# Performance work log

Hardware: AMD Instinct MI355X
Metric: run time of the kernel (lower is better)

Reference implementation:

```python
import jax, jax.numpy as jnp
import numpy as np


def _he_scale(k, shape, fan_in):
    return jax.random.normal(k, shape, dtype=jnp.float32) * np.sqrt(2.0 / fan_in).astype(np.float32)


def setup_inputs() -> dict:
    key = jax.random.key(0)
    kx, kt, kp, kg, kf = jax.random.split(key, 5)
    B, H, W, C, D = 4, 64, 64, 256, 128
    x = jax.random.normal(kx, (B, H, W, C), dtype=jnp.float32)
    Wt = _he_scale(kt, (C, D), C)
    Wp = _he_scale(kp, (C, D), C)
    Wg = _he_scale(kg, (C, D), C)
    Wf = _he_scale(kf, (D, C), D)
    return {"x": x, "Wt": Wt, "Wp": Wp, "Wg": Wg, "Wf": Wf}


def _maxpool1d(z, pool_size=2, stride=1):
    # Keras MaxPool1D, padding='valid': output length = (N - pool_size)//stride + 1
    return jax.lax.reduce_window(
        z, -jnp.inf, jax.lax.max,
        window_dimensions=(1, pool_size, 1),
        window_strides=(1, stride, 1),
        padding='VALID')


def reference(x, Wt, Wp, Wg, Wf):
    B, H, W, C = x.shape
    D = Wt.shape[1]
    N = H * W
    # 1x1 conv projections == per-position matmuls
    theta = jnp.einsum('bhwc,cd->bhwd', x, Wt).reshape(B, N, D)   # [B,N,D]
    phi = jnp.einsum('bhwc,cd->bhwd', x, Wp).reshape(B, N, D)     # [B,N,D]
    g = jnp.einsum('bhwc,cd->bhwd', x, Wg).reshape(B, N, D)       # [B,N,D]
    # embedded mode: subsample phi and g (pool_size=2, strides=1) -> M = N-1
    phi = _maxpool1d(phi)                                          # [B,M,D]
    g = _maxpool1d(g)                                              # [B,M,D]
    # f = theta @ phi^T, softmax over keys (no scaling in embedded mode)
    f = jax.nn.softmax(jnp.einsum('bnd,bmd->bnm', theta, phi), axis=-1)  # [B,N,M]
    y = jnp.einsum('bnm,bmd->bnd', f, g).reshape(B, H, W, D)       # [B,H,W,D]
    # final 1x1 conv back to C channels + residual
    z = x + jnp.einsum('bhwd,dc->bhwc', y, Wf)
    return z
```

## Files before the change

kernel.cpp:

```cpp
#include <hip/hip_runtime.h>

#define B_  4
#define N_  4096
#define C_  256
#define D_  128
#define M_  4095
#define BN_ (B_ * N_)

typedef _Float16 half_t;
typedef __attribute__((ext_vector_type(8))) _Float16 half8;
typedef __attribute__((ext_vector_type(4))) _Float16 half4;
typedef __attribute__((ext_vector_type(4))) float f32x4;

#define MFMA16x16x32(A, B, C) __builtin_amdgcn_mfma_f32_16x16x32_f16(A, B, C, 0, 0, 0)
#define LOG2E 1.44269504088896f
#define RTHR  5.0f

#define SWZ(r, c) ((c) ^ (((r) & 7) << 3))

__global__ __launch_bounds__(256) void prep_kernel(
    const float* __restrict__ Wt, const float* __restrict__ Wp,
    const float* __restrict__ Wg, const float* __restrict__ Wf,
    half_t* __restrict__ WT_hi, half_t* __restrict__ WfT)
{
    const int idx = blockIdx.x * 256 + threadIdx.x;
    const int wsel = blockIdx.y;
    if (wsel < 3) {
        const float* __restrict__ W = (wsel == 0) ? Wt : (wsel == 1) ? Wp : Wg;
        const int d = idx >> 8, c = idx & 255;
        WT_hi[(size_t)wsel * 32768 + idx] = (half_t)W[(size_t)c * D_ + d];
    } else {
        const int c = idx >> 7, d = idx & 127;
        WfT[idx] = (half_t)Wf[(size_t)d * C_ + c];
    }
}

__global__ __launch_bounds__(256) void proj_kernel(
    const float* __restrict__ x, const half_t* __restrict__ WT_hi,
    half_t* __restrict__ theta, half_t* __restrict__ pphi,
    half_t* __restrict__ pgT)
{
    const int tid = threadIdx.x;
    const int lane = tid & 63;
    const int w = tid >> 6;
    const int lm = lane & 15;
    const int lq = lane >> 4;
    const int r0 = blockIdx.x * 64;
    const int which = blockIdx.y;
    const half_t* __restrict__ Wg_ = WT_hi + (size_t)which * 32768;

    __shared__ __align__(16) unsigned char lds_raw[18432];
    half_t (*Xh)[40]  = (half_t (*)[40])(lds_raw);
    half_t (*Whl)[40] = (half_t (*)[40])(lds_raw + 5120);

    f32x4 acc[8];
#pragma unroll
    for (int nb = 0; nb < 8; ++nb)
#pragma unroll
        for (int r = 0; r < 4; ++r) acc[nb][r] = 0.f;

    const int xr = tid >> 2, xc = (tid & 3) * 8;
    const int wr = tid >> 1, wc = (tid & 1) * 16;

    const float* xs = x + (size_t)(r0 + xr) * C_ + xc;
    const half_t* wsrc = Wg_ + (size_t)wr * 256 + wc;
    float4 xv0 = *(const float4*)&xs[0];
    float4 xv1 = *(const float4*)&xs[4];
    half8 wv0 = *(const half8*)&wsrc[0];
    half8 wv1 = *(const half8*)&wsrc[8];

    for (int kc = 0; kc < 8; ++kc) {
        half8 hi;
        hi[0] = (half_t)xv0.x; hi[1] = (half_t)xv0.y;
        hi[2] = (half_t)xv0.z; hi[3] = (half_t)xv0.w;
        hi[4] = (half_t)xv1.x; hi[5] = (half_t)xv1.y;
        hi[6] = (half_t)xv1.z; hi[7] = (half_t)xv1.w;
        half8 w0 = wv0, w1 = wv1;
        __syncthreads();
        *(half8*)&Xh[xr][xc] = hi;
        *(half8*)&Whl[wr][wc]     = w0;
        *(half8*)&Whl[wr][wc + 8] = w1;
        if (kc < 7) {
            xs += 32; wsrc += 32;
            xv0 = *(const float4*)&xs[0];
            xv1 = *(const float4*)&xs[4];
            wv0 = *(const half8*)&wsrc[0];
            wv1 = *(const half8*)&wsrc[8];
        }
        __syncthreads();

        half8 ah = *(const half8*)&Xh[w * 16 + lm][lq * 8];
#pragma unroll
        for (int nb = 0; nb < 8; ++nb) {
            half8 bh = *(const half8*)&Whl[nb * 16 + lm][lq * 8];
            acc[nb] = MFMA16x16x32(ah, bh, acc[nb]);
        }
    }

    if (which == 0) {
#pragma unroll
        for (int nb = 0; nb < 8; ++nb)
#pragma unroll
            for (int r = 0; r < 4; ++r)
                theta[(size_t)(r0 + w * 16 + lq * 4 + r) * D_ + nb * 16 + lm] =
                    (half_t)(acc[nb][r] * LOG2E);
        return;
    }

    __syncthreads();
    half_t (*LsT)[72] = (half_t (*)[72])(lds_raw);
#pragma unroll
    for (int nb = 0; nb < 8; ++nb) {
        const int d = nb * 16 + lm;
        const int m = w * 16 + lq * 4;
        half4 pk;
#pragma unroll
        for (int r = 0; r < 4; ++r) pk[r] = (half_t)acc[nb][r];
        *(half4*)&LsT[d][m] = pk;
    }
    if (tid < 128) {
        int rh = r0 + 64;
        if ((rh & (N_ - 1)) == 0) rh = r0 + 63;
        const float* xrow = x + (size_t)rh * C_;
        const half_t* wrow = Wg_ + (size_t)tid * 256;
        float s = 0.f;
#pragma unroll
        for (int c8 = 0; c8 < 32; ++c8) {
            half8 h = *(const half8*)&wrow[c8 * 8];
            float4 xa = *(const float4*)&xrow[c8 * 8];
            float4 xb = *(const float4*)&xrow[c8 * 8 + 4];
            s += xa.x * (float)h[0] + xa.y * (float)h[1]
               + xa.z * (float)h[2] + xa.w * (float)h[3]
               + xb.x * (float)h[4] + xb.y * (float)h[5]
               + xb.z * (float)h[6] + xb.w * (float)h[7];
        }
        LsT[tid][64] = (half_t)s;
    }
    __syncthreads();

    if (which == 1) {
        const int m = tid >> 2, dh = (tid & 3) * 32;
        half8 o[4];
#pragma unroll
        for (int j = 0; j < 32; ++j) {
            float v0 = (float)LsT[dh + j][m];
            float v1 = (float)LsT[dh + j][m + 1];
            o[j >> 3][j & 7] = (half_t)fmaxf(v0, v1);
        }
        half8* dst = (half8*)&pphi[(size_t)(r0 + m) * D_ + dh];
#pragma unroll
        for (int j = 0; j < 4; ++j) dst[j] = o[j];
    } else {
        const int d = tid >> 1, mh = (tid & 1) * 32;
        const int b = r0 / N_, m0 = r0 & (N_ - 1);
        half8 in[4];
#pragma unroll
        for (int j = 0; j < 4; ++j) in[j] = *(const half8*)&LsT[d][mh + j * 8];
        const half_t ext = LsT[d][mh + 32];
        half8 o[4];
#pragma unroll
        for (int j = 0; j < 32; ++j) {
            float v0 = (float)in[j >> 3][j & 7];
            float v1 = (j == 31) ? (float)ext : (float)in[(j + 1) >> 3][(j + 1) & 7];
            o[j >> 3][j & 7] = (half_t)fmaxf(v0, v1);
        }
        half8* dst = (half8*)&pgT[((size_t)b * D_ + d) * N_ + m0 + mh];
#pragma unroll
        for (int j = 0; j < 4; ++j) dst[j] = o[j];
    }
}

template<int KS>
__global__ __launch_bounds__(256, 3) void attn_kernel(
    const half_t* __restrict__ theta, const half_t* __restrict__ pphi,
    const half_t* __restrict__ pgT, half_t* __restrict__ ypart,
    float* __restrict__ mstat, float* __restrict__ lstat)
{
    const int TILES = 64 / KS;
    const int tid = threadIdx.x;
    const int lane = tid & 63;
    const int w = tid >> 6;
    const int lm = lane & 15;
    const int lq = lane >> 4;
    const int qt = blockIdx.x, ksb = blockIdx.y, b = blockIdx.z;
    const int q0 = qt * 128;
    const int kt0 = ksb * TILES, kt1 = kt0 + TILES;

    __shared__ half_t Ks[64][128];
    __shared__ half_t Gts[128][64];
    __shared__ half_t Ps[128][64];

    half8 qh[2][4];
#pragma unroll
    for (int nb = 0; nb < 2; ++nb) {
        const half_t* tr_ = theta + ((size_t)b * N_ + q0 + w * 32 + nb * 16 + lm) * D_;
#pragma unroll
        for (int k4 = 0; k4 < 4; ++k4)
            qh[nb][k4] = *(const half8*)(tr_ + k4 * 32 + lq * 8);
    }

    const int key = tid >> 2, ch = tid & 3;
    const int gdd = tid >> 1, gkh = tid & 1;
    const float4* ksrc = (const float4*)(pphi +
        ((size_t)b * N_ + kt0 * 64 + key) * D_ + ch * 32);
    const float4* gsrc = (const float4*)(pgT +
        ((size_t)b * D_ + gdd) * N_ + kt0 * 64 + gkh * 32);

    float m_i[2] = {-1e30f, -1e30f};
    float l_i[2] = {0.f, 0.f};
    f32x4 yacc[2][8];
#pragma unroll
    for (int mb = 0; mb < 2; ++mb)
#pragma unroll
        for (int dn = 0; dn < 8; ++dn)
#pragma unroll
            for (int r = 0; r < 4; ++r) yacc[mb][dn][r] = 0.f;

    for (int kt = kt0; kt < kt1; ++kt) {
        const int k0 = kt * 64;
        __syncthreads();
        {
            float4 a0 = ksrc[0], a1 = ksrc[1], a2 = ksrc[2], a3 = ksrc[3];
            float4 g0 = gsrc[0], g1 = gsrc[1], g2 = gsrc[2], g3 = gsrc[3];
            ksrc += 1024;
            gsrc += 8;
            *(float4*)&Ks[key][SWZ(key, ch * 32 +  0)] = a0;
            *(float4*)&Ks[key][SWZ(key, ch * 32 +  8)] = a1;
            *(float4*)&Ks[key][SWZ(key, ch * 32 + 16)] = a2;
            *(float4*)&Ks[key][SWZ(key, ch * 32 + 24)] = a3;
            *(float4*)&Gts[gdd][SWZ(gdd, gkh * 32 +  0)] = g0;
            *(float4*)&Gts[gdd][SWZ(gdd, gkh * 32 +  8)] = g1;
            *(float4*)&Gts[gdd][SWZ(gdd, gkh * 32 + 16)] = g2;
            *(float4*)&Gts[gdd][SWZ(gdd, gkh * 32 + 24)] = g3;
        }
        __syncthreads();

        f32x4 sc[4][2];
#pragma unroll
        for (int kb = 0; kb < 4; ++kb)
#pragma unroll
            for (int nb = 0; nb < 2; ++nb)
#pragma unroll
                for (int r = 0; r < 4; ++r) sc[kb][nb][r] = 0.f;
        __builtin_amdgcn_s_setprio(1);
#pragma unroll
        for (int kb = 0; kb < 4; ++kb) {
            const int krow = kb * 16 + lm;
#pragma unroll
            for (int k4 = 0; k4 < 4; ++k4) {
                half8 kf = *(const half8*)&Ks[krow][SWZ(krow, k4 * 32 + lq * 8)];
#pragma unroll
                for (int nb = 0; nb < 2; ++nb)
                    sc[kb][nb] = MFMA16x16x32(kf, qh[nb][k4], sc[kb][nb]);
            }
        }
        __builtin_amdgcn_s_setprio(0);
        if (k0 + 64 > M_) {
#pragma unroll
            for (int kb = 0; kb < 4; ++kb)
#pragma unroll
                for (int r = 0; r < 4; ++r)
                    if (k0 + kb * 16 + lq * 4 + r >= M_) {
                        sc[kb][0][r] = -1e30f; sc[kb][1][r] = -1e30f;
                    }
        }

        float mt[2];
#pragma unroll
        for (int nb = 0; nb < 2; ++nb) {
            float m0 = -1e30f;
#pragma unroll
            for (int kb = 0; kb < 4; ++kb)
#pragma unroll
                for (int r = 0; r < 4; ++r) m0 = fmaxf(m0, sc[kb][nb][r]);
            m0 = fmaxf(m0, __shfl_xor(m0, 16, 64));
            m0 = fmaxf(m0, __shfl_xor(m0, 32, 64));
            mt[nb] = m0;
        }
        const bool need0 = __any(mt[0] > m_i[0] + RTHR);
        const bool need1 = __any(mt[1] > m_i[1] + RTHR);
        float alphav[2] = {1.f, 1.f};
#pragma unroll
        for (int nb = 0; nb < 2; ++nb) {
            const bool need = nb ? need1 : need0;
            float mnew = m_i[nb];
            if (need) {
                mnew = fmaxf(m_i[nb], mt[nb]);
                alphav[nb] = exp2f(m_i[nb] - mnew);
                m_i[nb] = mnew;
            }
            float rs = 0.f;
            const int prow = w * 32 + nb * 16 + lm;
#pragma unroll
            for (int kb = 0; kb < 4; ++kb) {
                half4 pk;
#pragma unroll
                for (int r = 0; r < 4; ++r) {
                    float p = exp2f(sc[kb][nb][r] - mnew);
                    rs += p;
                    pk[r] = (half_t)p;
                }
                *(half4*)&Ps[prow][SWZ(prow, kb * 16 + lq * 4)] = pk;
            }
            l_i[nb] = l_i[nb] * alphav[nb] + rs;
        }
        if (need0) {
            float a_t[4];
#pragma unroll
            for (int r = 0; r < 4; ++r) a_t[r] = __shfl(alphav[0], lq * 4 + r, 16);
#pragma unroll
            for (int dn = 0; dn < 8; ++dn)
#pragma unroll
                for (int r = 0; r < 4; ++r) yacc[0][dn][r] *= a_t[r];
        }
        if (need1) {
            float a_t[4];
#pragma unroll
            for (int r = 0; r < 4; ++r) a_t[r] = __shfl(alphav[1], lq * 4 + r, 16);
#pragma unroll
            for (int dn = 0; dn < 8; ++dn)
#pragma unroll
                for (int r = 0; r < 4; ++r) yacc[1][dn][r] *= a_t[r];
        }

        half8 pf[2][2];
#pragma unroll
        for (int mb = 0; mb < 2; ++mb) {
            const int prow = w * 32 + mb * 16 + lm;
#pragma unroll
            for (int k2 = 0; k2 < 2; ++k2)
                pf[mb][k2] = *(const half8*)&Ps[prow][SWZ(prow, k2 * 32 + lq * 8)];
        }
        __builtin_amdgcn_s_setprio(1);
#pragma unroll
        for (int dn = 0; dn < 8; ++dn) {
            const int grow = dn * 16 + lm;
#pragma unroll
            for (int k2 = 0; k2 < 2; ++k2) {
                half8 gf = *(const half8*)&Gts[grow][SWZ(grow, k2 * 32 + lq * 8)];
                yacc[0][dn] = MFMA16x16x32(pf[0][k2], gf, yacc[0][dn]);
                yacc[1][dn] = MFMA16x16x32(pf[1][k2], gf, yacc[1][dn]);
            }
        }
        __builtin_amdgcn_s_setprio(0);
    }

#pragma unroll
    for (int nb = 0; nb < 2; ++nb) {
        l_i[nb] += __shfl_xor(l_i[nb], 16, 64);
        l_i[nb] += __shfl_xor(l_i[nb], 32, 64);
    }
    half_t* yp = ypart + ((size_t)ksb * BN_ + (size_t)b * N_) * D_;
#pragma unroll
    for (int mb = 0; mb < 2; ++mb)
#pragma unroll
        for (int dn = 0; dn < 8; ++dn)
#pragma unroll
            for (int r = 0; r < 4; ++r)
                yp[(size_t)(q0 + w * 32 + mb * 16 + lq * 4 + r) * D_ + dn * 16 + lm] =
                    (half_t)yacc[mb][dn][r];
    if (lq == 0) {
#pragma unroll
        for (int nb = 0; nb < 2; ++nb) {
            const int row = q0 + w * 32 + nb * 16 + lm;
            mstat[(size_t)ksb * BN_ + (size_t)b * N_ + row] = m_i[nb];
            lstat[(size_t)ksb * BN_ + (size_t)b * N_ + row] = l_i[nb];
        }
    }
}

template<int KS>
__global__ __launch_bounds__(256) void final_kernel(
    const half_t* __restrict__ ypart, const float* __restrict__ mstat,
    const float* __restrict__ lstat, const float* __restrict__ x,
    const half_t* __restrict__ WfT, float* __restrict__ out)
{
    const int tid = threadIdx.x;
    const int lane = tid & 63;
    const int w = tid >> 6;
    const int lm = lane & 15;
    const int lq = lane >> 4;
    const int r0 = blockIdx.x * 64;
    const int c0 = blockIdx.y * 128;

    __shared__ half_t Ys[64][128];
    __shared__ half_t Wfs[128][128];
    __shared__ float scl[KS][64];

    if (tid < 64) {
        const int row = r0 + tid;
        float mv[KS], lv[KS], wv[KS];
        float Mx = -1e30f;
#pragma unroll
        for (int s = 0; s < KS; ++s) {
            mv[s] = mstat[(size_t)s * BN_ + row];
            lv[s] = lstat[(size_t)s * BN_ + row];
            Mx = fmaxf(Mx, mv[s]);
        }
        float lsum = 0.f;
#pragma unroll
        for (int s = 0; s < KS; ++s) { wv[s] = exp2f(mv[s] - Mx); lsum += wv[s] * lv[s]; }
        const float inv = 1.f / lsum;
#pragma unroll
        for (int s = 0; s < KS; ++s) scl[s][tid] = wv[s] * inv;
    }
    {
        const int wc = tid >> 1, wd = (tid & 1) * 64;
        const half_t* wf = WfT + (size_t)(c0 + wc) * D_ + wd;
#pragma unroll
        for (int q = 0; q < 8; ++q)
            *(half8*)&Wfs[wc][SWZ(wc, wd + q * 8)] = *(const half8*)&wf[q * 8];
    }
    __syncthreads();

    {
        const int sr = tid >> 2;
        const int dd = (tid & 3) * 32;
        float ss[KS];
#pragma unroll
        for (int s = 0; s < KS; ++s) ss[s] = scl[s][sr];
        const size_t yb = (size_t)(r0 + sr) * D_ + dd;
        half8 o[4];
#pragma unroll
        for (int q = 0; q < 4; ++q) {
            float m[8];
#pragma unroll
            for (int j = 0; j < 8; ++j) m[j] = 0.f;
#pragma unroll
            for (int s = 0; s < KS; ++s) {
                half8 yv = *(const half8*)&ypart[(size_t)s * BN_ * D_ + yb + q * 8];
#pragma unroll
                for (int j = 0; j < 8; ++j) m[j] += ss[s] * (float)yv[j];
            }
#pragma unroll
            for (int j = 0; j < 8; ++j) o[q][j] = (half_t)m[j];
        }
#pragma unroll
        for (int q = 0; q < 4; ++q) *(half8*)&Ys[sr][SWZ(sr, dd + q * 8)] = o[q];
    }
    __syncthreads();

    f32x4 acc[8];
#pragma unroll
    for (int nb = 0; nb < 8; ++nb)
#pragma unroll
        for (int r = 0; r < 4; ++r) acc[nb][r] = 0.f;

    const int yrow = w * 16 + lm;
#pragma unroll
    for (int k4 = 0; k4 < 4; ++k4) {
        half8 af = *(const half8*)&Ys[yrow][SWZ(yrow, k4 * 32 + lq * 8)];
#pragma unroll
        for (int nb = 0; nb < 8; ++nb) {
            const int wrow = nb * 16 + lm;
            half8 bf = *(const half8*)&Wfs[wrow][SWZ(wrow, k4 * 32 + lq * 8)];
            acc[nb] = MFMA16x16x32(af, bf, acc[nb]);
        }
    }

#pragma unroll
    for (int nb = 0; nb < 8; ++nb)
#pragma unroll
        for (int r = 0; r < 4; ++r) {
            const int row = r0 + w * 16 + lq * 4 + r;
            const int col = c0 + nb * 16 + lm;
            out[(size_t)row * C_ + col] =
                acc[nb][r] + x[(size_t)row * C_ + col];
        }
}

extern "C" void kernel_launch(void* const* d_in, const int* in_sizes, int n_in,
                              void* d_out, int out_size, void* d_ws, size_t ws_size,
                              hipStream_t stream)
{
    const float* x  = (const float*)d_in[0];
    const float* Wt = (const float*)d_in[1];
    const float* Wp = (const float*)d_in[2];
    const float* Wg = (const float*)d_in[3];
    const float* Wf = (const float*)d_in[4];
    float* out = (float*)d_out;

    const size_t SEG = (size_t)BN_ * D_;

    const size_t need8 = (3 + 8) * SEG * 2 + (size_t)2 * 8 * BN_ * 4 + 131072 * 2;
    const int KS = (ws_size >= need8) ? 8 : 4;

    half_t* hb    = (half_t*)d_ws;
    half_t* theta = hb;
    half_t* pphi  = hb + SEG;
    half_t* pgT   = hb + 2 * SEG;
    half_t* ypart = hb + 3 * SEG;
    float*  mstat = (float*)(hb + (size_t)(3 + KS) * SEG);
    float*  lstat = mstat + (size_t)KS * BN_;
    half_t* WT_hi = (half_t*)(lstat + (size_t)KS * BN_);
    half_t* WfT   = WT_hi + 3 * 32768;

    prep_kernel<<<dim3(128, 4), 256, 0, stream>>>(Wt, Wp, Wg, Wf, WT_hi, WfT);
    proj_kernel<<<dim3(BN_ / 64, 3), 256, 0, stream>>>(x, WT_hi, theta, pphi, pgT);
    if (KS == 8) {
        attn_kernel<8><<<dim3(N_ / 128, 8, B_), 256, 0, stream>>>(
            theta, pphi, pgT, ypart, mstat, lstat);
        final_kernel<8><<<dim3(BN_ / 64, 2), 256, 0, stream>>>(
            ypart, mstat, lstat, x, WfT, out);
    } else {
        attn_kernel<4><<<dim3(N_ / 128, 4, B_), 256, 0, stream>>>(
            theta, pphi, pgT, ypart, mstat, lstat);
        final_kernel<4><<<dim3(BN_ / 64, 2), 256, 0, stream>>>(
            ypart, mstat, lstat, x, WfT, out);
    }
}
```

Baseline: 174.4 us.

## Double-buffer K/G tiles with async global-to-LDS loads in attention kernel

The attention kernel now keeps two LDS buffers for the key and transposed-value tiles and fills the next tile with direct global_load_lds 16-byte copies while the current tile is consumed, which drops one barrier per iteration. It also removes the occupancy hint of three blocks per CU and fixes the key split at 4 instead of choosing 8 when the workspace is large enough. The aim is to hide global load latency behind the MFMA work. In exchange LDS use per block goes up (about 80KB), which may cut occupancy, and the smaller split means fewer blocks in the grid.

```diff
diff --git a/kernel.cpp b/kernel.cpp
--- a/kernel.cpp
+++ b/kernel.cpp
@@ -6,6 +6,7 @@
 #define D_  128
 #define M_  4095
 #define BN_ (B_ * N_)
+#define KSPLIT 4
 
 typedef _Float16 half_t;
 typedef __attribute__((ext_vector_type(8))) _Float16 half8;
@@ -17,6 +18,12 @@
 #define RTHR  5.0f
 
 #define SWZ(r, c) ((c) ^ (((r) & 7) << 3))
+
+__device__ __forceinline__ void gld16(const void* g, void* l) {
+    __builtin_amdgcn_global_load_lds(
+        (const __attribute__((address_space(1))) unsigned char*)g,
+        (__attribute__((address_space(3))) unsigned char*)l, 16, 0, 0);
+}
 
 __global__ __launch_bounds__(256) void prep_kernel(
     const float* __restrict__ Wt, const float* __restrict__ Wp,
@@ -171,7 +178,7 @@
 }
 
 template<int KS>
-__global__ __launch_bounds__(256, 3) void attn_kernel(
+__global__ __launch_bounds__(256) void attn_kernel(
     const half_t* __restrict__ theta, const half_t* __restrict__ pphi,
     const half_t* __restrict__ pgT, half_t* __restrict__ ypart,
     float* __restrict__ mstat, float* __restrict__ lstat)
@@ -186,8 +193,8 @@
     const int q0 = qt * 128;
     const int kt0 = ksb * TILES, kt1 = kt0 + TILES;
 
-    __shared__ half_t Ks[64][128];
-    __shared__ half_t Gts[128][64];
+    __shared__ half_t Ks[2][64][128];
+    __shared__ half_t Gts[2][128][64];
     __shared__ half_t Ps[128][64];
 
     half8 qh[2][4];
@@ -199,12 +206,26 @@
             qh[nb][k4] = *(const half8*)(tr_ + k4 * 32 + lq * 8);
     }
 
-    const int key = tid >> 2, ch = tid & 3;
-    const int gdd = tid >> 1, gkh = tid & 1;
-    const float4* ksrc = (const float4*)(pphi +
-        ((size_t)b * N_ + kt0 * 64 + key) * D_ + ch * 32);
-    const float4* gsrc = (const float4*)(pgT +
-        ((size_t)b * D_ + gdd) * N_ + kt0 * 64 + gkh * 32);
+    const char* kbase = (const char*)(pphi + (size_t)b * N_ * D_);
+    const char* gbase = (const char*)(pgT + (size_t)b * D_ * N_);
+    const int rlo4 = lane >> 4;
+    const int kco  = (lane & 15) * 16;
+    const int rlo8 = lane >> 3;
+    const int gco  = ((lane & 7) * 16) ^ (rlo8 << 4);
+
+    auto stage = [&](int bf, int kt) {
+#pragma unroll
+        for (int i = 0; i < 4; ++i) {
+            const int r4 = w * 4 + i;
+            const int krow = r4 * 4 + rlo4;
+            gld16(kbase + (size_t)kt * 16384 + (size_t)krow * 256
+                        + (kco ^ ((krow & 7) << 4)),
+                  &Ks[bf][r4 * 4][0]);
+            const int gd = r4 * 8 + rlo8;
+            gld16(gbase + (size_t)gd * (N_ * 2) + (size_t)kt * 128 + gco,
+                  &Gts[bf][r4 * 8][0]);
+        }
+    };
 
     float m_i[2] = {-1e30f, -1e30f};
     float l_i[2] = {0.f, 0.f};
@@ -216,24 +237,14 @@
 #pragma unroll
             for (int r = 0; r < 4; ++r) yacc[mb][dn][r] = 0.f;
 
+    int cur = 0;
+    stage(0, kt0);
+    __syncthreads();
+
     for (int kt = kt0; kt < kt1; ++kt) {
         const int k0 = kt * 64;
-        __syncthreads();
-        {
-            float4 a0 = ksrc[0], a1 = ksrc[1], a2 = ksrc[2], a3 = ksrc[3];
-            float4 g0 = gsrc[0], g1 = gsrc[1], g2 = gsrc[2], g3 = gsrc[3];
-            ksrc += 1024;
-            gsrc += 8;
-            *(float4*)&Ks[key][SWZ(key, ch * 32 +  0)] = a0;
-            *(float4*)&Ks[key][SWZ(key, ch * 32 +  8)] = a1;
-            *(float4*)&Ks[key][SWZ(key, ch * 32 + 16)] = a2;
-            *(float4*)&Ks[key][SWZ(key, ch * 32 + 24)] = a3;
-            *(float4*)&Gts[gdd][SWZ(gdd, gkh * 32 +  0)] = g0;
-            *(float4*)&Gts[gdd][SWZ(gdd, gkh * 32 +  8)] = g1;
-            *(float4*)&Gts[gdd][SWZ(gdd, gkh * 32 + 16)] = g2;
-            *(float4*)&Gts[gdd][SWZ(gdd, gkh * 32 + 24)] = g3;
-        }
-        __syncthreads();
+        const bool has_next = (kt + 1 < kt1);
+        if (has_next) stage(cur ^ 1, kt + 1);
 
         f32x4 sc[4][2];
 #pragma unroll
@@ -248,7 +259,7 @@
             const int krow = kb * 16 + lm;
 #pragma unroll
             for (int k4 = 0; k4 < 4; ++k4) {
-                half8 kf = *(const half8*)&Ks[krow][SWZ(krow, k4 * 32 + lq * 8)];
+                half8 kf = *(const half8*)&Ks[cur][krow][SWZ(krow, k4 * 32 + lq * 8)];
 #pragma unroll
                 for (int nb = 0; nb < 2; ++nb)
                     sc[kb][nb] = MFMA16x16x32(kf, qh[nb][k4], sc[kb][nb]);
@@ -337,12 +348,17 @@
             const int grow = dn * 16 + lm;
 #pragma unroll
             for (int k2 = 0; k2 < 2; ++k2) {
-                half8 gf = *(const half8*)&Gts[grow][SWZ(grow, k2 * 32 + lq * 8)];
+                half8 gf = *(const half8*)&Gts[cur][grow][SWZ(grow, k2 * 32 + lq * 8)];
                 yacc[0][dn] = MFMA16x16x32(pf[0][k2], gf, yacc[0][dn]);
                 yacc[1][dn] = MFMA16x16x32(pf[1][k2], gf, yacc[1][dn]);
             }
         }
         __builtin_amdgcn_s_setprio(0);
+
+        if (has_next) {
+            __syncthreads();
+            cur ^= 1;
+        }
     }
 
 #pragma unroll
@@ -482,30 +498,20 @@
 
     const size_t SEG = (size_t)BN_ * D_;
 
-    const size_t need8 = (3 + 8) * SEG * 2 + (size_t)2 * 8 * BN_ * 4 + 131072 * 2;
-    const int KS = (ws_size >= need8) ? 8 : 4;
-
     half_t* hb    = (half_t*)d_ws;
     half_t* theta = hb;
     half_t* pphi  = hb + SEG;
     half_t* pgT   = hb + 2 * SEG;
     half_t* ypart = hb + 3 * SEG;
-    float*  mstat = (float*)(hb + (size_t)(3 + KS) * SEG);
-    float*  lstat = mstat + (size_t)KS * BN_;
-    half_t* WT_hi = (half_t*)(lstat + (size_t)KS * BN_);
+    float*  mstat = (float*)(hb + (size_t)(3 + KSPLIT) * SEG);
+    float*  lstat = mstat + (size_t)KSPLIT * BN_;
+    half_t* WT_hi = (half_t*)(lstat + (size_t)KSPLIT * BN_);
     half_t* WfT   = WT_hi + 3 * 32768;
 
     prep_kernel<<<dim3(128, 4), 256, 0, stream>>>(Wt, Wp, Wg, Wf, WT_hi, WfT);
     proj_kernel<<<dim3(BN_ / 64, 3), 256, 0, stream>>>(x, WT_hi, theta, pphi, pgT);
-    if (KS == 8) {
-        attn_kernel<8><<<dim3(N_ / 128, 8, B_), 256, 0, stream>>>(
-            theta, pphi, pgT, ypart, mstat, lstat);
-        final_kernel<8><<<dim3(BN_ / 64, 2), 256, 0, stream>>>(
-            ypart, mstat, lstat, x, WfT, out);
-    } else {
-        attn_kernel<4><<<dim3(N_ / 128, 4, B_), 256, 0, stream>>>(
-            theta, pphi, pgT, ypart, mstat, lstat);
-        final_kernel<4><<<dim3(BN_ / 64, 2), 256, 0, stream>>>(
-            ypart, mstat, lstat, x, WfT, out);
-    }
+    attn_kernel<KSPLIT><<<dim3(N_ / 128, KSPLIT, B_), 256, 0, stream>>>(
+        theta, pphi, pgT, ypart, mstat, lstat);
+    final_kernel<KSPLIT><<<dim3(BN_ / 64, 2), 256, 0, stream>>>(
+        ypart, mstat, lstat, x, WfT, out);
 }
```

After: 195.2 us. 11.9% more time.
